# Kernel tuning notes

Hardware: AMD Instinct MI355X
Metric: run time of the kernel (lower is better)

Reference implementation:

```python
import jax, jax.numpy as jnp
import numpy as np
from jax import lax

B, T, V, E, H, M = 512, 60, 50000, 300, 512, 256


def _lstm_final_h(x_emb, seqlen, kernel, bias):
    """BasicLSTMCell (gate order i,j,f,o; forget_bias=1.0) with dynamic_rnn
    sequence_length semantics: state stops updating at t >= seqlen.
    x_emb: [B, T, E]; returns final h: [B, H]."""
    b = x_emb.shape[0]
    h0 = jnp.zeros((b, H), x_emb.dtype)
    c0 = jnp.zeros((b, H), x_emb.dtype)

    def step(carry, inp):
        c, h = carry
        xt, t = inp
        z = jnp.concatenate([xt, h], axis=1) @ kernel + bias  # [B, 4H]
        i, j, f, o = jnp.split(z, 4, axis=1)
        nc = c * jax.nn.sigmoid(f + 1.0) + jax.nn.sigmoid(i) * jnp.tanh(j)
        nh = jnp.tanh(nc) * jax.nn.sigmoid(o)
        valid = (t < seqlen)[:, None]
        return (jnp.where(valid, nc, c), jnp.where(valid, nh, h)), None

    (c, h), _ = lax.scan(step, (c0, h0),
                         (jnp.swapaxes(x_emb, 0, 1), jnp.arange(T)))
    return h


def setup_inputs() -> dict:
    key = jax.random.key(0)
    ks = jax.random.split(key, 8)
    return {
        "input1": jax.random.randint(ks[0], (B, T), 0, V, dtype=jnp.int32),
        "input2": jax.random.randint(ks[1], (B, T), 0, V, dtype=jnp.int32),
        "seqlen1": jax.random.randint(ks[2], (B,), 1, T + 1, dtype=jnp.int32),
        "seqlen2": jax.random.randint(ks[3], (B,), 1, T + 1, dtype=jnp.int32),
        "embeddings": jax.random.normal(ks[4], (V, E), jnp.float32) * 0.1,
        "lstm_kernel": jax.random.normal(ks[5], (E + H, 4 * H), jnp.float32) * 0.02,
        "lstm_bias": jnp.zeros((4 * H,), jnp.float32),
        "W1": jax.random.normal(ks[6], (4 * (H + 1) + 1, M), jnp.float32) * 0.02,
        "b1": jnp.zeros((1, M), jnp.float32),
        "W2": jax.random.normal(ks[7], (M, 2), jnp.float32) * 0.02,
        "b2": jnp.zeros((1, 2), jnp.float32),
    }


def reference(input1, input2, seqlen1, seqlen2, embeddings,
              lstm_kernel, lstm_bias, W1, b1, W2, b2):
    x1 = embeddings[input1]  # [B, T, E]
    x2 = embeddings[input2]
    h1 = _lstm_final_h(x1, seqlen1, lstm_kernel, lstm_bias)  # [B, H]
    h2 = _lstm_final_h(x2, seqlen2, lstm_kernel, lstm_bias)
    len1 = (seqlen1.astype(jnp.float32) / float(T))[:, None]
    len2 = (seqlen2.astype(jnp.float32) / float(T))[:, None]
    h1 = jnp.concatenate([h1, len1], axis=1)  # [B, H+1]
    h2 = jnp.concatenate([h2, len2], axis=1)
    h_sub = h1 - h2
    h_dist = jnp.sum(h_sub * h_sub, axis=1, keepdims=True)  # [B, 1]
    h_mul = h1 * h2
    h_combined = jnp.concatenate([h1, h2, h_sub, h_dist, h_mul], axis=1)
    e1 = jax.nn.relu(h_combined @ W1 + b1)  # dropout keep_prob=1 -> identity
    preds = e1 @ W2 + b2  # [B, 2]
    return preds
```

## Files before the change

### kernel.cpp

```cpp
#include <hip/hip_runtime.h>
#include <hip/hip_bf16.h>

#define BATCH 512
#define TT 60
#define EDIM 300
#define HDIM 512
#define KREAL 812
#define KP 896
#define KP1 2112
#define MDIM 256

typedef __bf16 bf16x4 __attribute__((ext_vector_type(4)));
typedef __bf16 bf16x8 __attribute__((ext_vector_type(8)));
typedef float  f32x16 __attribute__((ext_vector_type(16)));

#define GLL16(g, l) __builtin_amdgcn_global_load_lds( \
    (const __attribute__((address_space(1))) void*)(g), \
    (__attribute__((address_space(3))) void*)(l), 16, 0, 0)

__device__ __forceinline__ float sigm(float x) {
    return 1.0f / (1.0f + __expf(-x));
}
__device__ __forceinline__ float tanh_fast(float x) {
    float e = __expf(-2.0f * fabsf(x));
    float r = (1.0f - e) / (1.0f + e);
    return x >= 0.0f ? r : -r;
}


__global__ __launch_bounds__(256) void prep_w(const float* __restrict__ kern,
                                              __bf16* __restrict__ wf) {
    __shared__ float tile[64][65];
    int bk = blockIdx.x % 14;
    int bn = blockIdx.x / 14;
    int k0 = bk * 64, n0 = bn * 64;
    int tid = threadIdx.x;
#pragma unroll
    for (int i = 0; i < 16; ++i) {
        int id = i * 256 + tid;
        int kk = id >> 6, nn = id & 63;
        int kg = k0 + kk;
        int src = (kg < 300) ? kg : (kg >= 384 ? kg - 84 : -1);
        tile[kk][nn] = (src >= 0) ? kern[(size_t)src * 2048 + n0 + nn] : 0.0f;
    }
    __syncthreads();
    int gate = n0 >> 9;
    int nt = gate >> 1;
#pragma unroll
    for (int i = 0; i < 2; ++i) {
        int id = i * 256 + tid;
        int nn = id >> 3, k8 = id & 7;
        bf16x8 hv, lv;
#pragma unroll
        for (int j = 0; j < 8; ++j) {
            float v = tile[k8 * 8 + j][nn];
            __bf16 h = (__bf16)v;
            hv[j] = h;
            lv[j] = (__bf16)(v - (float)h);
        }
        int cg = (((n0 & 511) >> 4) + (nn >> 4));
        int hc = nn & 15;
        int lzc = ((gate & 1) << 4) + hc;
        int kglob = k0 + k8 * 8;
        int c = kglob >> 7;
        int j = (kglob >> 4) & 7;
        int half = k8 & 1;
        size_t o = (size_t)cg * 114688 + c * 16384 + (j * 4 + nt * 2) * 512
                 + (half * 32 + lzc) * 8;
        *(bf16x8*)(wf + o) = hv;
        *(bf16x8*)(wf + o + 512) = lv;
    }
}

__global__ __launch_bounds__(256) void prep_w1(const float* __restrict__ W1,
                                               __bf16* __restrict__ w1h,
                                               __bf16* __restrict__ w1l) {
    __shared__ float tile[64][65];
    int bk = blockIdx.x % 33;
    int bn = blockIdx.x / 33;
    int k0 = bk * 64, n0 = bn * 64;
    int tid = threadIdx.x;
#pragma unroll
    for (int i = 0; i < 16; ++i) {
        int id = i * 256 + tid;
        int kk = id >> 6, nn = id & 63;
        int kg = k0 + kk;
        tile[kk][nn] = (kg < 2053) ? W1[(size_t)kg * MDIM + n0 + nn] : 0.0f;
    }
    __syncthreads();
#pragma unroll
    for (int i = 0; i < 2; ++i) {
        int id = i * 256 + tid;
        int nn = id >> 3, k8 = (id & 7) * 8;
        bf16x8 hv, lv;
#pragma unroll
        for (int j = 0; j < 8; ++j) {
            float v = tile[k8 + j][nn];
            __bf16 h = (__bf16)v;
            hv[j] = h;
            lv[j] = (__bf16)(v - (float)h);
        }
        size_t o = (size_t)(n0 + nn) * KP1 + k0 + k8;
        *(bf16x8*)(w1h + o) = hv;
        *(bf16x8*)(w1l + o) = lv;
    }
}

__device__ __forceinline__ void emb_unit(int tok, int rl, int rr, int bt,
                                         const float* __restrict__ emb,
                                         __bf16* __restrict__ Xfn) {
    const float* er = emb + (size_t)tok * EDIM + rr * 8;
    float4 f0 = *(const float4*)er;
    float4 f1 = (rr == 37) ? make_float4(0.f, 0.f, 0.f, 0.f)
                           : *(const float4*)(er + 4);
    float vv[8] = {f0.x, f0.y, f0.z, f0.w, f1.x, f1.y, f1.z, f1.w};
    bf16x8 hv, lv;
#pragma unroll
    for (int j = 0; j < 8; ++j) {
        __bf16 h = (__bf16)vv[j];
        hv[j] = h;
        lv[j] = (__bf16)(vv[j] - (float)h);
    }
    int ke = rr * 8;
    int c = ke >> 7, kl = ke & 127;
    int kg = kl >> 6, jj = (kl >> 4) & 3, half = (kl >> 3) & 1;
    int s = rl >> 5;
    size_t base = ((((size_t)bt * 4 + s) * 2 + kg) * 7 + c) * 4096 + jj * 1024
                + (half * 32 + (rl & 31)) * 8;
    *(bf16x8*)(Xfn + base) = hv;
    *(bf16x8*)(Xfn + base + 512) = lv;
}

__global__ __launch_bounds__(256) void prep_x0(const int* __restrict__ in1,
                                               const int* __restrict__ in2,
                                               const float* __restrict__ emb,
                                               __bf16* __restrict__ Xf) {
    __shared__ int tk[128];
    int bt = blockIdx.x >> 5, cg = blockIdx.x & 31;
    int tid = threadIdx.x;
    if (tid < 128) {
        int rg = bt * 128 + tid, b = rg & 511;
        tk[tid] = ((rg >> 9) ? in2 : in1)[b * TT];
    }
    __syncthreads();
    if (tid < 152) {
        int id = tid * 32 + cg;
        int rl = id / 38, rr = id - rl * 38;
        emb_unit(tk[rl], rl, rr, bt, emb, Xf);
    }
}

__global__ __launch_bounds__(512, 2) void lstm_step(
    int t,
    const int* __restrict__ in1, const int* __restrict__ in2,
    const int* __restrict__ sl1, const int* __restrict__ sl2,
    const float* __restrict__ emb, const float* __restrict__ bias,
    const __bf16* __restrict__ wf,
    const __bf16* __restrict__ Xf, __bf16* __restrict__ Xfn,
    float* __restrict__ h_state, float* __restrict__ c_state) {

    __shared__ __align__(16) __bf16 Bb[2][16384];
    __shared__ int toks2[128];

    int tid = threadIdx.x;
    int bt = blockIdx.x >> 5, cg = blockIdx.x & 31;
    int row0 = bt << 7;
    int w = tid >> 6, lane = tid & 63, l31 = lane & 31;
    int s = w >> 1, kg = w & 1;

    if (tid < 128) {
        int rg = row0 + tid, b = rg & 511;
        int tn = (t + 1 < TT) ? t + 1 : t;
        toks2[tid] = ((rg >> 9) ? in2 : in1)[b * TT + tn];
    }

    const __bf16* wb = wf + (size_t)cg * 114688;

    auto stageB = [&](int c, int buf) {
        int Tb = w * 4;
        const __bf16* src = wb + c * 16384 + Tb * 512 + lane * 8;
        __bf16* dst = &Bb[buf][Tb * 512 + lane * 8];
#pragma unroll
        for (int i = 0; i < 4; ++i)
            GLL16(src + i * 512, dst + i * 512);
    };

    const __bf16* Abase = Xf + ((((size_t)bt * 4 + s) * 2 + kg) * 7) * 4096
                        + lane * 8;

    f32x16 acc[2];
#pragma unroll
    for (int nt = 0; nt < 2; ++nt)
#pragma unroll
        for (int r = 0; r < 16; ++r) acc[nt][r] = 0.0f;

    bf16x8 aH[4], aL[4];
    stageB(0, 0);
#pragma unroll
    for (int jj = 0; jj < 4; ++jj) {
        aH[jj] = *(const bf16x8*)(Abase + jj * 1024);
        aL[jj] = *(const bf16x8*)(Abase + jj * 1024 + 512);
    }
    __syncthreads();

#pragma unroll
    for (int c = 0; c < 7; ++c) {
        int cur = c & 1;
        bf16x8 nH[4], nL[4];
        if (c < 6) {
            stageB(c + 1, 1 - cur);
            const __bf16* An = Abase + (c + 1) * 4096;
#pragma unroll
            for (int jj = 0; jj < 4; ++jj) {
                nH[jj] = *(const bf16x8*)(An + jj * 1024);
                nL[jj] = *(const bf16x8*)(An + jj * 1024 + 512);
            }
        }
#pragma unroll
        for (int jj = 0; jj < 4; ++jj) {
            int j = kg * 4 + jj;
#pragma unroll
            for (int nt = 0; nt < 2; ++nt) {
                int T0 = (j * 4 + nt * 2) * 512 + lane * 8;
                bf16x8 bh = *(const bf16x8*)(&Bb[cur][T0]);
                bf16x8 bl = *(const bf16x8*)(&Bb[cur][T0 + 512]);
                acc[nt] = __builtin_amdgcn_mfma_f32_32x32x16_bf16(aH[jj], bh, acc[nt], 0, 0, 0);
                acc[nt] = __builtin_amdgcn_mfma_f32_32x32x16_bf16(aH[jj], bl, acc[nt], 0, 0, 0);
                acc[nt] = __builtin_amdgcn_mfma_f32_32x32x16_bf16(aL[jj], bh, acc[nt], 0, 0, 0);
            }
        }
        if (c < 6) {
#pragma unroll
            for (int jj = 0; jj < 4; ++jj) { aH[jj] = nH[jj]; aL[jj] = nL[jj]; }
        }
        __syncthreads();
    }

    float* zs = (float*)&Bb[1][0];
    if (kg == 0) {
#pragma unroll
        for (int nt = 0; nt < 2; ++nt)
#pragma unroll
            for (int r = 0; r < 16; ++r) {
                int rl = s * 32 + (r & 3) + ((r >> 2) << 3) + ((lane >> 5) << 2);
                zs[rl * 64 + nt * 32 + l31] = acc[nt][r];
            }
    }
    __syncthreads();
    if (kg == 1) {
#pragma unroll
        for (int nt = 0; nt < 2; ++nt)
#pragma unroll
            for (int r = 0; r < 16; ++r) {
                int rl = s * 32 + (r & 3) + ((r >> 2) << 3) + ((lane >> 5) << 2);
                zs[rl * 64 + nt * 32 + l31] += acc[nt][r];
            }
    }
    __syncthreads();

    __bf16* zh = &Bb[0][0];
#pragma unroll
    for (int i = 0; i < 4; ++i) {
        int eid = i * 512 + tid;
        int hc16 = eid & 15;
        int rl = eid >> 4;
        int rg = row0 + rl;
        int hcol = (cg << 4) + hc16;
        float zi = zs[rl * 64 + hc16]      + bias[hcol];
        float zj = zs[rl * 64 + 16 + hc16] + bias[512 + hcol];
        float zf = zs[rl * 64 + 32 + hc16] + bias[1024 + hcol];
        float zo = zs[rl * 64 + 48 + hc16] + bias[1536 + hcol];
        size_t so = (size_t)rg * HDIM + hcol;
        float c_old = c_state[so];
        float h_old = h_state[so];
        int b = rg & 511;
        int sl = (rg >> 9) ? sl2[b] : sl1[b];
        float nc = c_old * sigm(zf + 1.0f) + sigm(zi) * tanh_fast(zj);
        float nh = tanh_fast(nc) * sigm(zo);
        bool valid = t < sl;
        float cs = valid ? nc : c_old;
        float hs = valid ? nh : h_old;
        c_state[so] = cs;
        h_state[so] = hs;
        __bf16 hh = (__bf16)hs;
        int grp = hc16 >> 3, e = hc16 & 7;
        zh[((0 + grp) * 128 + rl) * 8 + e] = hh;
        zh[((2 + grp) * 128 + rl) * 8 + e] = (__bf16)(hs - (float)hh);
    }
    __syncthreads();

    {
        int u = tid;
        int plane = u >> 9 ? 0 : 0;
        plane = u >> 8;
        int grp = (u >> 7) & 1;
        int rl = u & 127;
        bf16x8 val = *(const bf16x8*)(zh + u * 8);
        int s2 = rl >> 5;
        int c2 = 3 + (cg >> 3);
        int kg2 = (cg & 7) >> 2;
        int jj2 = cg & 3;
        size_t base = ((((size_t)bt * 4 + s2) * 2 + kg2) * 7 + c2) * 4096
                    + jj2 * 1024 + plane * 512 + (grp * 32 + (rl & 31)) * 8;
        *(bf16x8*)(Xfn + base) = val;
    }

    if (t + 1 < TT && tid < 152) {
        int id = tid * 32 + cg;
        int rl = id / 38, rr = id - rl * 38;
        emb_unit(toks2[rl], rl, rr, bt, emb, Xfn);
    }
}

__global__ __launch_bounds__(256) void head1(const float* __restrict__ h_state,
                                             const int* __restrict__ sl1,
                                             const int* __restrict__ sl2,
                                             __bf16* __restrict__ hch,
                                             __bf16* __restrict__ hcl) {
    int b = blockIdx.x;
    int tid = threadIdx.x;
    const float* h1 = h_state + (size_t)b * HDIM;
    const float* h2 = h_state + (size_t)(512 + b) * HDIM;
    size_t ro = (size_t)b * KP1;
    float l1 = (float)sl1[b] / (float)TT;
    float l2 = (float)sl2[b] / (float)TT;
    float part = 0.0f;
#pragma unroll
    for (int i = 0; i < 2; ++i) {
        int k = i * 256 + tid;
        float a = h1[k], c = h2[k];
        float sv = a - c;
        float mv = a * c;
        __bf16 xh;
        xh = (__bf16)a;  hch[ro + k] = xh;         hcl[ro + k] = (__bf16)(a - (float)xh);
        xh = (__bf16)c;  hch[ro + 513 + k] = xh;   hcl[ro + 513 + k] = (__bf16)(c - (float)xh);
        xh = (__bf16)sv; hch[ro + 1026 + k] = xh;  hcl[ro + 1026 + k] = (__bf16)(sv - (float)xh);
        xh = (__bf16)mv; hch[ro + 1540 + k] = xh;  hcl[ro + 1540 + k] = (__bf16)(mv - (float)xh);
        part += sv * sv;
    }
    __shared__ float red[4];
#pragma unroll
    for (int off = 32; off > 0; off >>= 1) part += __shfl_down(part, off, 64);
    if ((tid & 63) == 0) red[tid >> 6] = part;
    __syncthreads();
    if (tid == 0) {
        float d = red[0] + red[1] + red[2] + red[3];
        float ls = l1 - l2;
        d += ls * ls;
        float vals[5] = {l1, l2, ls, d, l1 * l2};
        int pos[5] = {512, 1025, 1538, 1539, 2052};
#pragma unroll
        for (int i = 0; i < 5; ++i) {
            __bf16 xh = (__bf16)vals[i];
            hch[ro + pos[i]] = xh;
            hcl[ro + pos[i]] = (__bf16)(vals[i] - (float)xh);
        }
    }
}

__global__ __launch_bounds__(512, 2) void head2m(
    const __bf16* __restrict__ hch, const __bf16* __restrict__ hcl,
    const __bf16* __restrict__ w1h, const __bf16* __restrict__ w1l,
    float* __restrict__ part) {

    __shared__ __align__(16) __bf16 Bb[2][64 * 512];

    int tid = threadIdx.x;
    int bx = blockIdx.x;
    int mt = bx >> 3;
    int n2 = (bx >> 2) & 1;
    int ks = bx & 3;
    int w = tid >> 6, lane = tid & 63, l31 = lane & 31;
    int half8 = (lane >> 5) << 3;
    int s = w >> 1, nh = w & 1;
    int kbase = ks * 528;

    int k8 = tid & 15;
    int jb = k8 >> 1;
    int rb = (tid >> 4) & 31;
    size_t gboff[8];
    int lo[8];
#pragma unroll
    for (int i = 0; i < 8; ++i) {
        int r = ((i & 3) << 5) + rb;
        int plane = i >> 2;
        int ng = n2 * 128 + r;
        gboff[i] = (size_t)ng * KP1 + k8 * 8;
        int nt = r >> 5;
        int colp = ((r & 31) + (jb << 2)) & 31;
        lo[i] = ((((jb << 2) + nt) << 1) + plane) * 512 + (colp + ((k8 & 1) << 5)) * 8;
    }

    const __bf16* Ah0 = hch + (size_t)(mt * 128 + s * 32 + l31) * KP1 + kbase + half8;
    const __bf16* Al0 = hcl + (size_t)(mt * 128 + s * 32 + l31) * KP1 + kbase + half8;

    bf16x8 rB[8];
    f32x16 acc[2];
#pragma unroll
    for (int nt = 0; nt < 2; ++nt)
#pragma unroll
        for (int r = 0; r < 16; ++r) acc[nt][r] = 0.0f;

#pragma unroll
    for (int i = 0; i < 8; ++i)
        rB[i] = *(const bf16x8*)(((i >= 4) ? w1l : w1h) + gboff[i] + kbase);
#pragma unroll
    for (int i = 0; i < 8; ++i) *(bf16x8*)(&Bb[0][lo[i]]) = rB[i];
    __syncthreads();

    for (int c = 0; c < 5; ++c) {
        int cur = c & 1;
        if (c < 4) {
            int k0 = kbase + (c + 1) * 128;
            bool tail = (c + 1 == 4);
#pragma unroll
            for (int i = 0; i < 8; ++i) {
                if (!tail || k8 < 2)
                    rB[i] = *(const bf16x8*)(((i >= 4) ? w1l : w1h) + gboff[i] + k0);
            }
        }
        int jmax = (c == 4) ? 1 : 8;
        for (int j = 0; j < jmax; ++j) {
            bf16x8 ah = *(const bf16x8*)(Ah0 + c * 128 + j * 16);
            bf16x8 al = *(const bf16x8*)(Al0 + c * 128 + j * 16);
            int cp = ((l31 + (j << 2)) & 31) + ((lane >> 5) << 5);
#pragma unroll
            for (int ntl = 0; ntl < 2; ++ntl) {
                int ntg = nh * 2 + ntl;
                const __bf16* bp = &Bb[cur][(((j << 2) + ntg) << 1) * 512 + cp * 8];
                bf16x8 bh = *(const bf16x8*)bp;
                bf16x8 bl = *(const bf16x8*)(bp + 512);
                acc[ntl] = __builtin_amdgcn_mfma_f32_32x32x16_bf16(ah, bh, acc[ntl], 0, 0, 0);
                acc[ntl] = __builtin_amdgcn_mfma_f32_32x32x16_bf16(ah, bl, acc[ntl], 0, 0, 0);
                acc[ntl] = __builtin_amdgcn_mfma_f32_32x32x16_bf16(al, bh, acc[ntl], 0, 0, 0);
            }
        }
        if (c < 4) {
#pragma unroll
            for (int i = 0; i < 8; ++i) *(bf16x8*)(&Bb[1 - cur][lo[i]]) = rB[i];
        }
        __syncthreads();
    }

#pragma unroll
    for (int ntl = 0; ntl < 2; ++ntl)
#pragma unroll
        for (int r = 0; r < 16; ++r) {
            int row = mt * 128 + s * 32 + (r & 3) + ((r >> 2) << 3) + ((lane >> 5) << 2);
            int col = n2 * 128 + nh * 64 + ntl * 32 + l31;
            part[((size_t)ks * 512 + row) * MDIM + col] = acc[ntl][r];
        }
}

__global__ __launch_bounds__(256) void head3(const float* __restrict__ part,
                                             const float* __restrict__ b1,
                                             const float* __restrict__ W2,
                                             const float* __restrict__ b2,
                                             float* __restrict__ out) {
    int row = blockIdx.x;
    int tid = threadIdx.x;
    float sv = b1[tid];
#pragma unroll
    for (int ks = 0; ks < 4; ++ks)
        sv += part[((size_t)ks * 512 + row) * MDIM + tid];
    float e = fmaxf(sv, 0.0f);
    float p0 = e * W2[tid * 2 + 0];
    float p1 = e * W2[tid * 2 + 1];
#pragma unroll
    for (int off = 32; off > 0; off >>= 1) {
        p0 += __shfl_down(p0, off, 64);
        p1 += __shfl_down(p1, off, 64);
    }
    __shared__ float r0[4], r1[4];
    if ((tid & 63) == 0) { r0[tid >> 6] = p0; r1[tid >> 6] = p1; }
    __syncthreads();
    if (tid == 0) out[row * 2 + 0] = r0[0] + r0[1] + r0[2] + r0[3] + b2[0];
    if (tid == 1) out[row * 2 + 1] = r1[0] + r1[1] + r1[2] + r1[3] + b2[1];
}

extern "C" void kernel_launch(void* const* d_in, const int* in_sizes, int n_in,
                              void* d_out, int out_size, void* d_ws, size_t ws_size,
                              hipStream_t stream) {
    const int*   in1  = (const int*)d_in[0];
    const int*   in2  = (const int*)d_in[1];
    const int*   sl1  = (const int*)d_in[2];
    const int*   sl2  = (const int*)d_in[3];
    const float* emb  = (const float*)d_in[4];
    const float* kern = (const float*)d_in[5];
    const float* bias = (const float*)d_in[6];
    const float* W1   = (const float*)d_in[7];
    const float* b1   = (const float*)d_in[8];
    const float* W2   = (const float*)d_in[9];
    const float* b2   = (const float*)d_in[10];
    float* out = (float*)d_out;

    char* ws = (char*)d_ws;
    float*  c_state = (float*)ws;
    float*  h_state = (float*)(ws + 2097152u);
    __bf16* Xf0 = (__bf16*)(ws + 4194304u);
    __bf16* Xf1 = (__bf16*)(ws + 7864320u);
    __bf16* wf  = (__bf16*)(ws + 11534336u);
    __bf16* hch = (__bf16*)(ws + 18874368u);
    __bf16* hcl = (__bf16*)(ws + 21037056u);
    __bf16* w1h = (__bf16*)(ws + 23199744u);
    __bf16* w1l = (__bf16*)(ws + 24281088u);
    float*  part = (float*)(ws + 25362432u);

    hipMemsetAsync(ws, 0, 11534336u, stream);
    hipMemsetAsync(ws + 18874368u, 0, 4325376u, stream);

    prep_w<<<dim3(14 * 32), dim3(256), 0, stream>>>(kern, wf);
    prep_w1<<<dim3(33 * 4), dim3(256), 0, stream>>>(W1, w1h, w1l);
    prep_x0<<<dim3(256), dim3(256), 0, stream>>>(in1, in2, emb, Xf0);

    for (int t = 0; t < TT; ++t) {
        __bf16* Xf  = (t & 1) ? Xf1 : Xf0;
        __bf16* Xfn = (t & 1) ? Xf0 : Xf1;
        lstm_step<<<dim3(256), dim3(512), 0, stream>>>(
            t, in1, in2, sl1, sl2, emb, bias, wf, Xf, Xfn, h_state, c_state);
    }

    head1<<<dim3(512), dim3(256), 0, stream>>>(h_state, sl1, sl2, hch, hcl);
    head2m<<<dim3(32), dim3(512), 0, stream>>>(hch, hcl, w1h, w1l, part);
    head3<<<dim3(512), dim3(256), 0, stream>>>(part, b1, W2, b2, out);
}
```

Measured before the change: 1.296 ms.

## Fuse all LSTM timesteps into one persistent kernel with grid barriers

```diff
diff --git a/kernel.cpp b/kernel.cpp
--- a/kernel.cpp
+++ b/kernel.cpp
@@ -108,7 +108,7 @@
 
 __device__ __forceinline__ void emb_unit(int tok, int rl, int rr, int bt,
                                          const float* __restrict__ emb,
-                                         __bf16* __restrict__ Xfn) {
+                                         __bf16* Xfn) {
     const float* er = emb + (size_t)tok * EDIM + rr * 8;
     float4 f0 = *(const float4*)er;
     float4 f1 = (rr == 37) ? make_float4(0.f, 0.f, 0.f, 0.f)
@@ -150,16 +150,30 @@
     }
 }
 
-__global__ __launch_bounds__(512, 2) void lstm_step(
-    int t,
+__device__ __forceinline__ void gridbar(unsigned* ctr, int tid) {
+    __syncthreads();
+    if (tid == 0) {
+        __threadfence();
+        atomicAdd(ctr, 1u);
+        while (__hip_atomic_load(ctr, __ATOMIC_ACQUIRE,
+                                 __HIP_MEMORY_SCOPE_AGENT) < 256u)
+            __builtin_amdgcn_s_sleep(8);
+        __threadfence();
+    }
+    __syncthreads();
+}
+
+__global__ __launch_bounds__(512, 2) void lstm_all(
     const int* __restrict__ in1, const int* __restrict__ in2,
     const int* __restrict__ sl1, const int* __restrict__ sl2,
     const float* __restrict__ emb, const float* __restrict__ bias,
     const __bf16* __restrict__ wf,
-    const __bf16* __restrict__ Xf, __bf16* __restrict__ Xfn,
-    float* __restrict__ h_state, float* __restrict__ c_state) {
+    __bf16* Xf0, __bf16* Xf1,
+    float* __restrict__ h_state, unsigned* bar) {
 
     __shared__ __align__(16) __bf16 Bb[2][16384];
+    __shared__ float zs[128 * 64];
+    __shared__ __bf16 zh[4 * 128 * 8];
     __shared__ int toks2[128];
 
     int tid = threadIdx.x;
@@ -168,13 +182,22 @@
     int w = tid >> 6, lane = tid & 63, l31 = lane & 31;
     int s = w >> 1, kg = w & 1;
 
-    if (tid < 128) {
-        int rg = row0 + tid, b = rg & 511;
-        int tn = (t + 1 < TT) ? t + 1 : t;
-        toks2[tid] = ((rg >> 9) ? in2 : in1)[b * TT + tn];
-    }
-
     const __bf16* wb = wf + (size_t)cg * 114688;
+
+    int rloc = tid >> 4;
+    int hc16 = tid & 15;
+    int hcol = (cg << 4) + hc16;
+    float creg[4] = {0.f, 0.f, 0.f, 0.f};
+    float hreg[4] = {0.f, 0.f, 0.f, 0.f};
+    float bi = bias[hcol], bj = bias[512 + hcol];
+    float bf = bias[1024 + hcol], bo = bias[1536 + hcol];
+    int slr[4];
+#pragma unroll
+    for (int i = 0; i < 4; ++i) {
+        int rg = row0 + i * 32 + rloc;
+        int b = rg & 511;
+        slr[i] = (rg >> 9) ? sl2[b] : sl1[b];
+    }
 
     auto stageB = [&](int c, int buf) {
         int Tb = w * 4;
@@ -185,130 +208,135 @@
             GLL16(src + i * 512, dst + i * 512);
     };
 
-    const __bf16* Abase = Xf + ((((size_t)bt * 4 + s) * 2 + kg) * 7) * 4096
-                        + lane * 8;
-
-    f32x16 acc[2];
-#pragma unroll
-    for (int nt = 0; nt < 2; ++nt)
-#pragma unroll
-        for (int r = 0; r < 16; ++r) acc[nt][r] = 0.0f;
-
-    bf16x8 aH[4], aL[4];
     stageB(0, 0);
-#pragma unroll
-    for (int jj = 0; jj < 4; ++jj) {
-        aH[jj] = *(const bf16x8*)(Abase + jj * 1024);
-        aL[jj] = *(const bf16x8*)(Abase + jj * 1024 + 512);
-    }
-    __syncthreads();
-
-#pragma unroll
-    for (int c = 0; c < 7; ++c) {
-        int cur = c & 1;
-        bf16x8 nH[4], nL[4];
-        if (c < 6) {
-            stageB(c + 1, 1 - cur);
-            const __bf16* An = Abase + (c + 1) * 4096;
+
+    for (int t = 0; t < TT; ++t) {
+        const __bf16* Xf = (t & 1) ? Xf1 : Xf0;
+        __bf16* Xfn = (t & 1) ? Xf0 : Xf1;
+
+        if (tid < 128) {
+            int rg = row0 + tid, b = rg & 511;
+            int tn = (t + 1 < TT) ? t + 1 : t;
+            toks2[tid] = ((rg >> 9) ? in2 : in1)[b * TT + tn];
+        }
+
+        const __bf16* Abase = Xf + ((((size_t)bt * 4 + s) * 2 + kg) * 7) * 4096
+                            + lane * 8;
+
+        f32x16 acc[2];
+#pragma unroll
+        for (int nt = 0; nt < 2; ++nt)
+#pragma unroll
+            for (int r = 0; r < 16; ++r) acc[nt][r] = 0.0f;
+
+        bf16x8 aH[4], aL[4];
+#pragma unroll
+        for (int jj = 0; jj < 4; ++jj) {
+            aH[jj] = *(const bf16x8*)(Abase + jj * 1024);
+            aL[jj] = *(const bf16x8*)(Abase + jj * 1024 + 512);
+        }
+        __syncthreads();
+
+#pragma unroll
+        for (int c = 0; c < 7; ++c) {
+            int cur = c & 1;
+            bf16x8 nH[4], nL[4];
+            if (c < 6) {
+                stageB(c + 1, 1 - cur);
+                const __bf16* An = Abase + (c + 1) * 4096;
+#pragma unroll
+                for (int jj = 0; jj < 4; ++jj) {
+                    nH[jj] = *(const bf16x8*)(An + jj * 1024);
+                    nL[jj] = *(const bf16x8*)(An + jj * 1024 + 512);
+                }
+            }
 #pragma unroll
             for (int jj = 0; jj < 4; ++jj) {
-                nH[jj] = *(const bf16x8*)(An + jj * 1024);
-                nL[jj] = *(const bf16x8*)(An + jj * 1024 + 512);
-            }
-        }
-#pragma unroll
-        for (int jj = 0; jj < 4; ++jj) {
-            int j = kg * 4 + jj;
-#pragma unroll
-            for (int nt = 0; nt < 2; ++nt) {
-                int T0 = (j * 4 + nt * 2) * 512 + lane * 8;
-                bf16x8 bh = *(const bf16x8*)(&Bb[cur][T0]);
-                bf16x8 bl = *(const bf16x8*)(&Bb[cur][T0 + 512]);
-                acc[nt] = __builtin_amdgcn_mfma_f32_32x32x16_bf16(aH[jj], bh, acc[nt], 0, 0, 0);
-                acc[nt] = __builtin_amdgcn_mfma_f32_32x32x16_bf16(aH[jj], bl, acc[nt], 0, 0, 0);
-                acc[nt] = __builtin_amdgcn_mfma_f32_32x32x16_bf16(aL[jj], bh, acc[nt], 0, 0, 0);
-            }
-        }
-        if (c < 6) {
-#pragma unroll
-            for (int jj = 0; jj < 4; ++jj) { aH[jj] = nH[jj]; aL[jj] = nL[jj]; }
+                int j = kg * 4 + jj;
+#pragma unroll
+                for (int nt = 0; nt < 2; ++nt) {
+                    int T0 = (j * 4 + nt * 2) * 512 + lane * 8;
+                    bf16x8 bh = *(const bf16x8*)(&Bb[cur][T0]);
+                    bf16x8 bl = *(const bf16x8*)(&Bb[cur][T0 + 512]);
+                    acc[nt] = __builtin_amdgcn_mfma_f32_32x32x16_bf16(aH[jj], bh, acc[nt], 0, 0, 0);
+                    acc[nt] = __builtin_amdgcn_mfma_f32_32x32x16_bf16(aH[jj], bl, acc[nt], 0, 0, 0);
+                    acc[nt] = __builtin_amdgcn_mfma_f32_32x32x16_bf16(aL[jj], bh, acc[nt], 0, 0, 0);
+                }
+            }
+            if (c < 6) {
+#pragma unroll
+                for (int jj = 0; jj < 4; ++jj) { aH[jj] = nH[jj]; aL[jj] = nL[jj]; }
+            }
+            __syncthreads();
+        }
+
+        if (kg == 0) {
+#pragma unroll
+            for (int nt = 0; nt < 2; ++nt)
+#pragma unroll
+                for (int r = 0; r < 16; ++r) {
+                    int rl = s * 32 + (r & 3) + ((r >> 2) << 3) + ((lane >> 5) << 2);
+                    zs[rl * 64 + nt * 32 + l31] = acc[nt][r];
+                }
         }
         __syncthreads();
-    }
-
-    float* zs = (float*)&Bb[1][0];
-    if (kg == 0) {
-#pragma unroll
-        for (int nt = 0; nt < 2; ++nt)
-#pragma unroll
-            for (int r = 0; r < 16; ++r) {
-                int rl = s * 32 + (r & 3) + ((r >> 2) << 3) + ((lane >> 5) << 2);
-                zs[rl * 64 + nt * 32 + l31] = acc[nt][r];
-            }
-    }
-    __syncthreads();
-    if (kg == 1) {
-#pragma unroll
-        for (int nt = 0; nt < 2; ++nt)
-#pragma unroll
-            for (int r = 0; r < 16; ++r) {
-                int rl = s * 32 + (r & 3) + ((r >> 2) << 3) + ((lane >> 5) << 2);
-                zs[rl * 64 + nt * 32 + l31] += acc[nt][r];
-            }
-    }
-    __syncthreads();
-
-    __bf16* zh = &Bb[0][0];
-#pragma unroll
-    for (int i = 0; i < 4; ++i) {
-        int eid = i * 512 + tid;
-        int hc16 = eid & 15;
-        int rl = eid >> 4;
-        int rg = row0 + rl;
-        int hcol = (cg << 4) + hc16;
-        float zi = zs[rl * 64 + hc16]      + bias[hcol];
-        float zj = zs[rl * 64 + 16 + hc16] + bias[512 + hcol];
-        float zf = zs[rl * 64 + 32 + hc16] + bias[1024 + hcol];
-        float zo = zs[rl * 64 + 48 + hc16] + bias[1536 + hcol];
-        size_t so = (size_t)rg * HDIM + hcol;
-        float c_old = c_state[so];
-        float h_old = h_state[so];
-        int b = rg & 511;
-        int sl = (rg >> 9) ? sl2[b] : sl1[b];
-        float nc = c_old * sigm(zf + 1.0f) + sigm(zi) * tanh_fast(zj);
-        float nh = tanh_fast(nc) * sigm(zo);
-        bool valid = t < sl;
-        float cs = valid ? nc : c_old;
-        float hs = valid ? nh : h_old;
-        c_state[so] = cs;
-        h_state[so] = hs;
-        __bf16 hh = (__bf16)hs;
-        int grp = hc16 >> 3, e = hc16 & 7;
-        zh[((0 + grp) * 128 + rl) * 8 + e] = hh;
-        zh[((2 + grp) * 128 + rl) * 8 + e] = (__bf16)(hs - (float)hh);
-    }
-    __syncthreads();
-
-    {
-        int u = tid;
-        int plane = u >> 9 ? 0 : 0;
-        plane = u >> 8;
-        int grp = (u >> 7) & 1;
-        int rl = u & 127;
-        bf16x8 val = *(const bf16x8*)(zh + u * 8);
-        int s2 = rl >> 5;
-        int c2 = 3 + (cg >> 3);
-        int kg2 = (cg & 7) >> 2;
-        int jj2 = cg & 3;
-        size_t base = ((((size_t)bt * 4 + s2) * 2 + kg2) * 7 + c2) * 4096
-                    + jj2 * 1024 + plane * 512 + (grp * 32 + (rl & 31)) * 8;
-        *(bf16x8*)(Xfn + base) = val;
-    }
-
-    if (t + 1 < TT && tid < 152) {
-        int id = tid * 32 + cg;
-        int rl = id / 38, rr = id - rl * 38;
-        emb_unit(toks2[rl], rl, rr, bt, emb, Xfn);
+        if (kg == 1) {
+#pragma unroll
+            for (int nt = 0; nt < 2; ++nt)
+#pragma unroll
+                for (int r = 0; r < 16; ++r) {
+                    int rl = s * 32 + (r & 3) + ((r >> 2) << 3) + ((lane >> 5) << 2);
+                    zs[rl * 64 + nt * 32 + l31] += acc[nt][r];
+                }
+        }
+        __syncthreads();
+
+#pragma unroll
+        for (int i = 0; i < 4; ++i) {
+            int rl = i * 32 + rloc;
+            float zi = zs[rl * 64 + hc16]      + bi;
+            float zj = zs[rl * 64 + 16 + hc16] + bj;
+            float zf = zs[rl * 64 + 32 + hc16] + bf;
+            float zo = zs[rl * 64 + 48 + hc16] + bo;
+            float nc = creg[i] * sigm(zf + 1.0f) + sigm(zi) * tanh_fast(zj);
+            float nh = tanh_fast(nc) * sigm(zo);
+            bool valid = t < slr[i];
+            creg[i] = valid ? nc : creg[i];
+            hreg[i] = valid ? nh : hreg[i];
+            __bf16 hh = (__bf16)hreg[i];
+            int grp = hc16 >> 3, e = hc16 & 7;
+            zh[((0 + grp) * 128 + rl) * 8 + e] = hh;
+            zh[((2 + grp) * 128 + rl) * 8 + e] = (__bf16)(hreg[i] - (float)hh);
+        }
+        __syncthreads();
+
+        if (t + 1 < TT) {
+            {
+                int u = tid;
+                int plane = u >> 8;
+                int grp = (u >> 7) & 1;
+                int rl = u & 127;
+                bf16x8 val = *(const bf16x8*)(zh + u * 8);
+                int s2 = rl >> 5;
+                int c2 = 3 + (cg >> 3);
+                int kg2 = (cg & 7) >> 2;
+                int jj2 = cg & 3;
+                size_t base = ((((size_t)bt * 4 + s2) * 2 + kg2) * 7 + c2) * 4096
+                            + jj2 * 1024 + plane * 512 + (grp * 32 + (rl & 31)) * 8;
+                *(bf16x8*)(Xfn + base) = val;
+            }
+            if (tid < 152) {
+                int id = tid * 32 + cg;
+                int rl = id / 38, rr = id - rl * 38;
+                emb_unit(toks2[rl], rl, rr, bt, emb, Xfn);
+            }
+            stageB(0, 0);
+            gridbar(bar + t, tid);
+        } else {
+#pragma unroll
+            for (int i = 0; i < 4; ++i)
+                h_state[(size_t)(row0 + i * 32 + rloc) * HDIM + hcol] = hreg[i];
+        }
     }
 }
 
@@ -495,7 +523,7 @@
     float* out = (float*)d_out;
 
     char* ws = (char*)d_ws;
-    float*  c_state = (float*)ws;
+    unsigned* bar = (unsigned*)ws;
     float*  h_state = (float*)(ws + 2097152u);
     __bf16* Xf0 = (__bf16*)(ws + 4194304u);
     __bf16* Xf1 = (__bf16*)(ws + 7864320u);
@@ -513,12 +541,8 @@
     prep_w1<<<dim3(33 * 4), dim3(256), 0, stream>>>(W1, w1h, w1l);
     prep_x0<<<dim3(256), dim3(256), 0, stream>>>(in1, in2, emb, Xf0);
 
-    for (int t = 0; t < TT; ++t) {
-        __bf16* Xf  = (t & 1) ? Xf1 : Xf0;
-        __bf16* Xfn = (t & 1) ? Xf0 : Xf1;
-        lstm_step<<<dim3(256), dim3(512), 0, stream>>>(
-            t, in1, in2, sl1, sl2, emb, bias, wf, Xf, Xfn, h_state, c_state);
-    }
+    lstm_all<<<dim3(256), dim3(512), 0, stream>>>(
+        in1, in2, sl1, sl2, emb, bias, wf, Xf0, Xf1, h_state, bar);
 
     head1<<<dim3(512), dim3(256), 0, stream>>>(h_state, sl1, sl2, hch, hcl);
     head2m<<<dim3(32), dim3(512), 0, stream>>>(hch, hcl, w1h, w1l, part);
```

Result: slower. 2.504 ms (+93.3%).

## Sort rows by sequence length and skip finished row tiles per step

Applied to the files above, without the earlier changes.

```diff
diff --git a/kernel.cpp b/kernel.cpp
--- a/kernel.cpp
+++ b/kernel.cpp
@@ -27,6 +27,38 @@
     return x >= 0.0f ? r : -r;
 }
 
+
+__global__ __launch_bounds__(256) void sort_rows(const int* __restrict__ sl1,
+                                                 const int* __restrict__ sl2,
+                                                 int* __restrict__ rowinfo,
+                                                 unsigned* __restrict__ nact) {
+    __shared__ unsigned cnt[61];
+    __shared__ unsigned off[61];
+    int tid = threadIdx.x;
+    if (tid < 61) cnt[tid] = 0;
+    __syncthreads();
+    for (int i = tid; i < 1024; i += 256) {
+        int sl = (i < 512) ? sl1[i] : sl2[i - 512];
+        atomicAdd(&cnt[60 - sl], 1u);
+    }
+    __syncthreads();
+    if (tid == 0) {
+        unsigned s = 0;
+        for (int k = 0; k < 61; ++k) { off[k] = s; s += cnt[k]; }
+        for (int t = 0; t < 60; ++t) {
+            unsigned act = off[60 - t];
+            nact[t] = (act + 63) >> 6;
+        }
+    }
+    __syncthreads();
+    for (int i = tid; i < 1024; i += 256) {
+        int sc = i >= 512;
+        int b = i & 511;
+        int sl = sc ? sl2[b] : sl1[b];
+        unsigned pos = atomicAdd(&off[60 - sl], 1u);
+        rowinfo[pos] = b | (sc << 15) | (sl << 20);
+    }
+}
 
 __global__ __launch_bounds__(256) void prep_w(const float* __restrict__ kern,
                                               __bf16* __restrict__ wf) {
@@ -108,7 +140,7 @@
 
 __device__ __forceinline__ void emb_unit(int tok, int rl, int rr, int bt,
                                          const float* __restrict__ emb,
-                                         __bf16* __restrict__ Xfn) {
+                                         __bf16* Xfn) {
     const float* er = emb + (size_t)tok * EDIM + rr * 8;
     float4 f0 = *(const float4*)er;
     float4 f1 = (rr == 37) ? make_float4(0.f, 0.f, 0.f, 0.f)
@@ -125,7 +157,7 @@
     int c = ke >> 7, kl = ke & 127;
     int kg = kl >> 6, jj = (kl >> 4) & 3, half = (kl >> 3) & 1;
     int s = rl >> 5;
-    size_t base = ((((size_t)bt * 4 + s) * 2 + kg) * 7 + c) * 4096 + jj * 1024
+    size_t base = ((((size_t)bt * 2 + s) * 2 + kg) * 7 + c) * 4096 + jj * 1024
                 + (half * 32 + (rl & 31)) * 8;
     *(bf16x8*)(Xfn + base) = hv;
     *(bf16x8*)(Xfn + base + 512) = lv;
@@ -133,59 +165,65 @@
 
 __global__ __launch_bounds__(256) void prep_x0(const int* __restrict__ in1,
                                                const int* __restrict__ in2,
+                                               const int* __restrict__ rowinfo,
                                                const float* __restrict__ emb,
                                                __bf16* __restrict__ Xf) {
-    __shared__ int tk[128];
+    __shared__ int tk[64];
     int bt = blockIdx.x >> 5, cg = blockIdx.x & 31;
     int tid = threadIdx.x;
-    if (tid < 128) {
-        int rg = bt * 128 + tid, b = rg & 511;
-        tk[tid] = ((rg >> 9) ? in2 : in1)[b * TT];
-    }
-    __syncthreads();
-    if (tid < 152) {
+    if (tid < 64) {
+        int info = rowinfo[bt * 64 + tid];
+        int b = info & 511, sc = (info >> 15) & 1;
+        tk[tid] = (sc ? in2 : in1)[b * TT];
+    }
+    __syncthreads();
+    if (tid < 76) {
         int id = tid * 32 + cg;
         int rl = id / 38, rr = id - rl * 38;
         emb_unit(tk[rl], rl, rr, bt, emb, Xf);
     }
 }
 
-__global__ __launch_bounds__(512, 2) void lstm_step(
+#define ZSTR 72
+
+__global__ __launch_bounds__(256, 2) void lstm_step(
     int t,
     const int* __restrict__ in1, const int* __restrict__ in2,
-    const int* __restrict__ sl1, const int* __restrict__ sl2,
+    const int* __restrict__ rowinfo, const unsigned* __restrict__ nact,
     const float* __restrict__ emb, const float* __restrict__ bias,
     const __bf16* __restrict__ wf,
     const __bf16* __restrict__ Xf, __bf16* __restrict__ Xfn,
     float* __restrict__ h_state, float* __restrict__ c_state) {
 
+    int bt = blockIdx.x >> 5, cg = blockIdx.x & 31;
+    if (bt >= (int)nact[t]) return;
+
     __shared__ __align__(16) __bf16 Bb[2][16384];
-    __shared__ int toks2[128];
-
-    int tid = threadIdx.x;
-    int bt = blockIdx.x >> 5, cg = blockIdx.x & 31;
-    int row0 = bt << 7;
+    __shared__ int info_s[64];
+    __shared__ int tk[64];
+
+    int tid = threadIdx.x;
     int w = tid >> 6, lane = tid & 63, l31 = lane & 31;
     int s = w >> 1, kg = w & 1;
 
-    if (tid < 128) {
-        int rg = row0 + tid, b = rg & 511;
+    if (tid < 64) {
+        int info = rowinfo[bt * 64 + tid];
+        info_s[tid] = info;
+        int b = info & 511, sc = (info >> 15) & 1;
         int tn = (t + 1 < TT) ? t + 1 : t;
-        toks2[tid] = ((rg >> 9) ? in2 : in1)[b * TT + tn];
+        tk[tid] = (sc ? in2 : in1)[b * TT + tn];
     }
 
     const __bf16* wb = wf + (size_t)cg * 114688;
-
     auto stageB = [&](int c, int buf) {
-        int Tb = w * 4;
-        const __bf16* src = wb + c * 16384 + Tb * 512 + lane * 8;
-        __bf16* dst = &Bb[buf][Tb * 512 + lane * 8];
-#pragma unroll
-        for (int i = 0; i < 4; ++i)
+        const __bf16* src = wb + c * 16384 + w * 4096 + lane * 8;
+        __bf16* dst = &Bb[buf][w * 4096 + lane * 8];
+#pragma unroll
+        for (int i = 0; i < 8; ++i)
             GLL16(src + i * 512, dst + i * 512);
     };
 
-    const __bf16* Abase = Xf + ((((size_t)bt * 4 + s) * 2 + kg) * 7) * 4096
+    const __bf16* Abase = Xf + ((((size_t)bt * 2 + s) * 2 + kg) * 7) * 4096
                         + lane * 8;
 
     f32x16 acc[2];
@@ -243,7 +281,7 @@
 #pragma unroll
             for (int r = 0; r < 16; ++r) {
                 int rl = s * 32 + (r & 3) + ((r >> 2) << 3) + ((lane >> 5) << 2);
-                zs[rl * 64 + nt * 32 + l31] = acc[nt][r];
+                zs[rl * ZSTR + nt * 32 + l31] = acc[nt][r];
             }
     }
     __syncthreads();
@@ -253,62 +291,60 @@
 #pragma unroll
             for (int r = 0; r < 16; ++r) {
                 int rl = s * 32 + (r & 3) + ((r >> 2) << 3) + ((lane >> 5) << 2);
-                zs[rl * 64 + nt * 32 + l31] += acc[nt][r];
+                zs[rl * ZSTR + nt * 32 + l31] += acc[nt][r];
             }
     }
     __syncthreads();
 
     __bf16* zh = &Bb[0][0];
+    int hc16 = tid & 15;
+    int hcol = (cg << 4) + hc16;
+    float bi = bias[hcol], bj = bias[512 + hcol];
+    float bfv = bias[1024 + hcol], bo = bias[1536 + hcol];
 #pragma unroll
     for (int i = 0; i < 4; ++i) {
-        int eid = i * 512 + tid;
-        int hc16 = eid & 15;
-        int rl = eid >> 4;
-        int rg = row0 + rl;
-        int hcol = (cg << 4) + hc16;
-        float zi = zs[rl * 64 + hc16]      + bias[hcol];
-        float zj = zs[rl * 64 + 16 + hc16] + bias[512 + hcol];
-        float zf = zs[rl * 64 + 32 + hc16] + bias[1024 + hcol];
-        float zo = zs[rl * 64 + 48 + hc16] + bias[1536 + hcol];
-        size_t so = (size_t)rg * HDIM + hcol;
-        float c_old = c_state[so];
-        float h_old = h_state[so];
-        int b = rg & 511;
-        int sl = (rg >> 9) ? sl2[b] : sl1[b];
+        int rl = i * 16 + (tid >> 4);
+        int info = info_s[rl];
+        int b = info & 511, sc = (info >> 15) & 1, sl = info >> 20;
+        float zi = zs[rl * ZSTR + hc16]      + bi;
+        float zj = zs[rl * ZSTR + 16 + hc16] + bj;
+        float zf = zs[rl * ZSTR + 32 + hc16] + bfv;
+        float zo = zs[rl * ZSTR + 48 + hc16] + bo;
+        size_t co = (size_t)(bt * 64 + rl) * HDIM + hcol;
+        size_t ho = (size_t)((sc << 9) + b) * HDIM + hcol;
+        float c_old = c_state[co];
+        float h_old = h_state[ho];
         float nc = c_old * sigm(zf + 1.0f) + sigm(zi) * tanh_fast(zj);
         float nh = tanh_fast(nc) * sigm(zo);
         bool valid = t < sl;
         float cs = valid ? nc : c_old;
         float hs = valid ? nh : h_old;
-        c_state[so] = cs;
-        h_state[so] = hs;
+        c_state[co] = cs;
+        h_state[ho] = hs;
         __bf16 hh = (__bf16)hs;
         int grp = hc16 >> 3, e = hc16 & 7;
-        zh[((0 + grp) * 128 + rl) * 8 + e] = hh;
-        zh[((2 + grp) * 128 + rl) * 8 + e] = (__bf16)(hs - (float)hh);
-    }
-    __syncthreads();
-
-    {
-        int u = tid;
-        int plane = u >> 9 ? 0 : 0;
-        plane = u >> 8;
-        int grp = (u >> 7) & 1;
-        int rl = u & 127;
-        bf16x8 val = *(const bf16x8*)(zh + u * 8);
+        zh[(grp * 64 + rl) * 8 + e] = hh;
+        zh[((2 + grp) * 64 + rl) * 8 + e] = (__bf16)(hs - (float)hh);
+    }
+    __syncthreads();
+
+    if (t + 1 < TT) {
+        int plane = tid >> 7;
+        int grp = (tid >> 6) & 1;
+        int rl = tid & 63;
+        bf16x8 val = *(const bf16x8*)(zh + ((plane * 2 + grp) * 64 + rl) * 8);
         int s2 = rl >> 5;
         int c2 = 3 + (cg >> 3);
-        int kg2 = (cg & 7) >> 2;
+        int kg2 = (cg >> 2) & 1;
         int jj2 = cg & 3;
-        size_t base = ((((size_t)bt * 4 + s2) * 2 + kg2) * 7 + c2) * 4096
+        size_t base = ((((size_t)bt * 2 + s2) * 2 + kg2) * 7 + c2) * 4096
                     + jj2 * 1024 + plane * 512 + (grp * 32 + (rl & 31)) * 8;
         *(bf16x8*)(Xfn + base) = val;
-    }
-
-    if (t + 1 < TT && tid < 152) {
-        int id = tid * 32 + cg;
-        int rl = id / 38, rr = id - rl * 38;
-        emb_unit(toks2[rl], rl, rr, bt, emb, Xfn);
+        if (tid < 76) {
+            int id = tid * 32 + cg;
+            int rl2 = id / 38, rr = id - rl2 * 38;
+            emb_unit(tk[rl2], rl2, rr, bt, emb, Xfn);
+        }
     }
 }
 
@@ -495,29 +531,33 @@
     float* out = (float*)d_out;
 
     char* ws = (char*)d_ws;
-    float*  c_state = (float*)ws;
+    int*      rowinfo = (int*)ws;
+    unsigned* nact    = (unsigned*)(ws + 4096u);
     float*  h_state = (float*)(ws + 2097152u);
-    __bf16* Xf0 = (__bf16*)(ws + 4194304u);
-    __bf16* Xf1 = (__bf16*)(ws + 7864320u);
-    __bf16* wf  = (__bf16*)(ws + 11534336u);
-    __bf16* hch = (__bf16*)(ws + 18874368u);
-    __bf16* hcl = (__bf16*)(ws + 21037056u);
-    __bf16* w1h = (__bf16*)(ws + 23199744u);
-    __bf16* w1l = (__bf16*)(ws + 24281088u);
-    float*  part = (float*)(ws + 25362432u);
-
-    hipMemsetAsync(ws, 0, 11534336u, stream);
-    hipMemsetAsync(ws + 18874368u, 0, 4325376u, stream);
-
+    float*  c_state = (float*)(ws + 4194304u);
+    __bf16* Xf0 = (__bf16*)(ws + 6291456u);
+    __bf16* Xf1 = (__bf16*)(ws + 9961472u);
+    __bf16* wf  = (__bf16*)(ws + 13631488u);
+    __bf16* hch = (__bf16*)(ws + 20971520u);
+    __bf16* hcl = (__bf16*)(ws + 23134208u);
+    __bf16* w1h = (__bf16*)(ws + 25296896u);
+    __bf16* w1l = (__bf16*)(ws + 26378240u);
+    float*  part = (float*)(ws + 27459584u);
+
+    hipMemsetAsync(ws + 2097152u, 0, 11534336u, stream);
+    hipMemsetAsync(ws + 20971520u, 0, 4325376u, stream);
+
+    sort_rows<<<dim3(1), dim3(256), 0, stream>>>(sl1, sl2, rowinfo, nact);
     prep_w<<<dim3(14 * 32), dim3(256), 0, stream>>>(kern, wf);
     prep_w1<<<dim3(33 * 4), dim3(256), 0, stream>>>(W1, w1h, w1l);
-    prep_x0<<<dim3(256), dim3(256), 0, stream>>>(in1, in2, emb, Xf0);
+    prep_x0<<<dim3(512), dim3(256), 0, stream>>>(in1, in2, rowinfo, emb, Xf0);
 
     for (int t = 0; t < TT; ++t) {
         __bf16* Xf  = (t & 1) ? Xf1 : Xf0;
         __bf16* Xfn = (t & 1) ? Xf0 : Xf1;
-        lstm_step<<<dim3(256), dim3(512), 0, stream>>>(
-            t, in1, in2, sl1, sl2, emb, bias, wf, Xf, Xfn, h_state, c_state);
+        lstm_step<<<dim3(512), dim3(256), 0, stream>>>(
+            t, in1, in2, rowinfo, nact, emb, bias, wf, Xf, Xfn,
+            h_state, c_state);
     }
 
     head1<<<dim3(512), dim3(256), 0, stream>>>(h_state, sl1, sl2, hch, hcl);
```

Measured after the change: 1.126 ms. 1.15x faster.
